# Optimization experiments

Measured on AMD Instinct MI355X. Metric: run time of the kernel, lower is better.

The kernel has to match this reference:

```python
import jax, jax.numpy as jnp
import numpy as np

EPS = 1e-06

def _feature_map(x):
    # elu(x) + 1
    return jax.nn.elu(x) + 1.0

def setup_inputs() -> dict:
    key = jax.random.key(0)
    k1, k2, k3 = jax.random.split(key, 3)
    N, L, H, D = 4, 8192, 8, 128
    queries = jax.random.normal(k1, (N, L, H, D), dtype=jnp.float32)
    keys = jax.random.normal(k2, (N, L, H, D), dtype=jnp.float32)
    values = jax.random.normal(k3, (N, L, H, D), dtype=jnp.float32)
    threshold = jnp.array([0.1], dtype=jnp.float32)
    return {"queries": queries, "keys": keys, "values": values, "threshold": threshold}

def reference(queries, keys, values, threshold):
    Q = _feature_map(queries)            # [N,L,H,D]
    K = _feature_map(keys)               # [N,L,H,D]
    v_length = values.shape[1]
    v = values / v_length                # [N,L,H,V]
    KV = jnp.einsum('nshd,nshv->nhdv', K, v)            # [N,H,D,V]
    scores = jnp.einsum('nlhd,nhd->nlh', Q, K.sum(axis=1))  # [N,L,H]
    sparse = jnp.where(scores > threshold[0], scores, jnp.zeros_like(scores))
    Z = 1.0 / (sparse + EPS)             # [N,L,H]
    out = jnp.einsum('nlhd,nhdv,nlh->nlhv', Q, KV, Z) * v_length
    return out
```

## Files before the change

kernel.cpp:

```cpp
#include <hip/hip_runtime.h>
#include <stdint.h>


#define LSEQ 8192
#define NHD  1024

typedef __attribute__((ext_vector_type(4))) float f32x4;
typedef __attribute__((ext_vector_type(8))) short bf16x8;
typedef unsigned short ushort_t;

static __device__ __forceinline__ unsigned short f2bf(float x) {
  union { float f; uint32_t u; } v; v.f = x;
  uint32_t r = v.u + 0x7FFFu + ((v.u >> 16) & 1u);
  return (unsigned short)(r >> 16);
}
static __device__ __forceinline__ uint32_t pack_bf(float a, float b) {
  return (uint32_t)f2bf(a) | ((uint32_t)f2bf(b) << 16);
}
static __device__ __forceinline__ float featmap(float x) {
  return x > 0.f ? x + 1.f : __expf(x);
}

#define LPAD 136

__global__ __launch_bounds__(512) void kv_direct(const float* __restrict__ keys,
                                                 const float* __restrict__ values,
                                                 float* __restrict__ kvp,
                                                 float* __restrict__ kspart) {
  __shared__ float kls[32 * LPAD];
  __shared__ float vls[32 * LPAD];
  const int tid = threadIdx.x;
  const int chunk = blockIdx.x, CH = gridDim.x;
  const int h = blockIdx.y, n = blockIdx.z, nh = n * 8 + h;
  const int lane = tid & 63, w = tid >> 6;
  const int wr = w >> 2, wc = w & 3;
  const int lr = lane & 15, lg = lane >> 4;
  const int sPer = LSEQ / CH;
  const int steps = sPer / 32;

  const size_t gb = ((size_t)n * LSEQ + (size_t)chunk * sPer) * NHD + h * 128;
  const float* gk = keys + gb;
  const float* gv = values + gb;

  const int srow = tid >> 5;
  const int c4 = tid & 31;

  f32x4 acc[4][2] = {};
  f32x4 ak[4] = {};
  bf16x8 ones;
  { uint32_t* u = (uint32_t*)&ones; u[0] = u[1] = u[2] = u[3] = 0x3F803F80u; }

  float4 kr[2], vr[2];
#pragma unroll
  for (int it = 0; it < 2; ++it) {
    size_t off = (size_t)(it * 16 + srow) * NHD + c4 * 4;
    kr[it] = *(const float4*)(gk + off);
    vr[it] = *(const float4*)(gv + off);
  }

  for (int t = 0; t < steps; ++t) {
#pragma unroll
    for (int it = 0; it < 2; ++it) {
      int s = it * 16 + srow;
      float4 kf = kr[it];
      kf.x = featmap(kf.x); kf.y = featmap(kf.y);
      kf.z = featmap(kf.z); kf.w = featmap(kf.w);
      *(float4*)&kls[s * LPAD + c4 * 4] = kf;
      *(float4*)&vls[s * LPAD + c4 * 4] = vr[it];
    }
    __syncthreads();
    if (t + 1 < steps) {
#pragma unroll
      for (int it = 0; it < 2; ++it) {
        size_t off = (size_t)((t + 1) * 32 + it * 16 + srow) * NHD + c4 * 4;
        kr[it] = *(const float4*)(gk + off);
        vr[it] = *(const float4*)(gv + off);
      }
    }
    bf16x8 af[4], bfr[2];
#pragma unroll
    for (int fr = 0; fr < 4; ++fr) {
      int d = wr * 64 + fr * 16 + lr;
      float f[8];
#pragma unroll
      for (int j = 0; j < 8; ++j) f[j] = kls[(lg * 8 + j) * LPAD + d];
      uint32_t* u = (uint32_t*)&af[fr];
      u[0] = pack_bf(f[0], f[1]); u[1] = pack_bf(f[2], f[3]);
      u[2] = pack_bf(f[4], f[5]); u[3] = pack_bf(f[6], f[7]);
    }
#pragma unroll
    for (int fc = 0; fc < 2; ++fc) {
      int v = wc * 32 + fc * 16 + lr;
      float f[8];
#pragma unroll
      for (int j = 0; j < 8; ++j) f[j] = vls[(lg * 8 + j) * LPAD + v];
      uint32_t* u = (uint32_t*)&bfr[fc];
      u[0] = pack_bf(f[0], f[1]); u[1] = pack_bf(f[2], f[3]);
      u[2] = pack_bf(f[4], f[5]); u[3] = pack_bf(f[6], f[7]);
    }
#pragma unroll
    for (int fr = 0; fr < 4; ++fr)
#pragma unroll
      for (int fc = 0; fc < 2; ++fc)
        acc[fr][fc] = __builtin_amdgcn_mfma_f32_16x16x32_bf16(af[fr], bfr[fc], acc[fr][fc], 0, 0, 0);
    if (wc == 0) {
#pragma unroll
      for (int fr = 0; fr < 4; ++fr)
        ak[fr] = __builtin_amdgcn_mfma_f32_16x16x32_bf16(af[fr], ones, ak[fr], 0, 0, 0);
    }
    __syncthreads();
  }

  float* dst = kvp + ((size_t)chunk * 32 + nh) * 16384;
#pragma unroll
  for (int fr = 0; fr < 4; ++fr)
#pragma unroll
    for (int fc = 0; fc < 2; ++fc) {
      int d0 = wr * 64 + fr * 16 + lg * 4;
      int v  = wc * 32 + fc * 16 + lr;
      *(float4*)(dst + (size_t)v * 128 + d0) =
          make_float4(acc[fr][fc][0], acc[fr][fc][1], acc[fr][fc][2], acc[fr][fc][3]);
    }
  if (wc == 0 && lr == 0) {
    float* ks = kspart + ((size_t)chunk * 32 + nh) * 128;
#pragma unroll
    for (int fr = 0; fr < 4; ++fr)
      *(float4*)(ks + wr * 64 + fr * 16 + lg * 4) =
          make_float4(ak[fr][0], ak[fr][1], ak[fr][2], ak[fr][3]);
  }
}

__global__ __launch_bounds__(256) void kv_merge(const float* __restrict__ kvp,
                                                const float* __restrict__ kspart,
                                                ushort_t* __restrict__ kvb,
                                                float* __restrict__ ksumg,
                                                int CH) {
  const int nh = blockIdx.x, q = blockIdx.y, tid = threadIdx.x;
  const size_t off = (size_t)nh * 16384 + q * 4096;
#pragma unroll
  for (int i = 0; i < 4; ++i) {
    size_t idx = off + (size_t)(i * 256 + tid) * 4;
    f32x4 s = {};
    for (int c = 0; c < CH; ++c)
      s += *(const f32x4*)(kvp + (size_t)c * 524288 + idx);
    *(uint2*)(kvb + idx) = make_uint2(pack_bf(s[0], s[1]), pack_bf(s[2], s[3]));
  }
  if (q == 0 && tid < 128) {
    float s = 0.f;
    for (int c = 0; c < CH; ++c) s += kspart[((size_t)c * 32 + nh) * 128 + tid];
    ksumg[nh * 128 + tid] = s;
  }
}

__global__ __launch_bounds__(256, 4) void attn_out(const float* __restrict__ q,
                                                   const ushort_t* __restrict__ kvb,
                                                   const float* __restrict__ ksumg,
                                                   const float* __restrict__ thrp,
                                                   float* __restrict__ out) {
  __shared__ __align__(16) uint32_t As[128 * 17 * 4];
  __shared__ float zrow[128];

  const int tid = threadIdx.x;
  const int mc = blockIdx.x, nh = blockIdx.y;
  const int n = nh >> 3, h = nh & 7;
  const size_t qoff = ((size_t)(n * LSEQ + mc * 128)) * NHD + h * 128;
  const float thr = thrp[0];

  const int c4 = tid & 31;
  const float4 kk = *(const float4*)(ksumg + nh * 128 + c4 * 4);

#pragma unroll
  for (int it = 0; it < 16; ++it) {
    int rr = it * 8 + (tid >> 5);
    float4 qv = *(const float4*)(q + qoff + (size_t)rr * NHD + c4 * 4);
    float f0 = featmap(qv.x), f1 = featmap(qv.y), f2 = featmap(qv.z), f3 = featmap(qv.w);
    uint32_t* dst = &As[(rr * 17 + (c4 >> 1)) * 4 + (c4 & 1) * 2];
    dst[0] = pack_bf(f0, f1);
    dst[1] = pack_bf(f2, f3);
    float p = f0 * kk.x + f1 * kk.y + f2 * kk.z + f3 * kk.w;
    p += __shfl_xor(p, 1);  p += __shfl_xor(p, 2);  p += __shfl_xor(p, 4);
    p += __shfl_xor(p, 8);  p += __shfl_xor(p, 16);
    if (c4 == 0) {
      float sp = p > thr ? p : 0.f;
      zrow[rr] = 1.f / (sp + 1e-6f);
    }
  }
  __syncthreads();

  const int lane = tid & 63;
  const int w = tid >> 6;
  const int lr = lane & 15, lg = lane >> 4;
  const ushort_t* kvp = kvb + (size_t)nh * 16384;

  f32x4 acc0[8] = {};
  f32x4 acc1[8] = {};
#pragma unroll
  for (int ks = 0; ks < 4; ++ks) {
    const int c8 = ks * 4 + lg;
    const int dof = ks * 32 + lg * 8;
    const int r0 = w * 32 + lr;
    bf16x8 a0 = *(const bf16x8*)&As[(r0 * 17 + c8) * 4];
    bf16x8 a1 = *(const bf16x8*)&As[((r0 + 16) * 17 + c8) * 4];
#pragma unroll
    for (int ct = 0; ct < 8; ++ct) {
      bf16x8 bb = *(const bf16x8*)(kvp + (size_t)((ct * 16 + lr) * 128) + dof);
      acc0[ct] = __builtin_amdgcn_mfma_f32_16x16x32_bf16(a0, bb, acc0[ct], 0, 0, 0);
      acc1[ct] = __builtin_amdgcn_mfma_f32_16x16x32_bf16(a1, bb, acc1[ct], 0, 0, 0);
    }
  }

  float z0[4], z1[4];
#pragma unroll
  for (int j = 0; j < 4; ++j) {
    z0[j] = zrow[w * 32 + lg * 4 + j];
    z1[j] = zrow[w * 32 + 16 + lg * 4 + j];
  }
  float* op = out + qoff;
#pragma unroll
  for (int ct = 0; ct < 8; ++ct)
#pragma unroll
    for (int jj = 0; jj < 4; ++jj) {
      int row = w * 32 + lg * 4 + jj;
      op[(size_t)row * NHD + ct * 16 + lr]        = acc0[ct][jj] * z0[jj];
      op[(size_t)(row + 16) * NHD + ct * 16 + lr] = acc1[ct][jj] * z1[jj];
    }
}

extern "C" void kernel_launch(void* const* d_in, const int* in_sizes, int n_in,
                              void* d_out, int out_size, void* d_ws, size_t ws_size,
                              hipStream_t stream) {
  const float* queries   = (const float*)d_in[0];
  const float* keys      = (const float*)d_in[1];
  const float* values    = (const float*)d_in[2];
  const float* threshold = (const float*)d_in[3];
  float* out = (float*)d_out;

  int CH = 16;
  while (CH > 1 &&
         (size_t)CH * (524288 + 32 * 128) * 4 + (size_t)32 * 16384 * 2 + 32 * 128 * 4 > ws_size)
    CH >>= 1;
  float* kvp     = (float*)d_ws;
  float* kspart  = kvp + (size_t)CH * 524288;
  ushort_t* kvb  = (ushort_t*)(kspart + (size_t)CH * 32 * 128);
  float* ksumg   = (float*)(kvb + (size_t)32 * 16384);

  kv_direct<<<dim3(CH, 8, 4), 512, 0, stream>>>(keys, values, kvp, kspart);
  kv_merge<<<dim3(32, 4), 256, 0, stream>>>(kvp, kspart, kvb, ksumg, CH);
  attn_out<<<dim3(64, 32), 256, 0, stream>>>(queries, kvb, ksumg, threshold, out);
}
```

Baseline: 193.9 us.

## Store K/V tiles in LDS as pre-packed transposed bf16 with XOR swizzle

The K/V tiles are now converted to bf16 and transposed (feature-major) before being written to shared memory. An XOR swizzle and padded stride are meant to avoid bank conflicts. Each MFMA operand then comes from a single 16-byte LDS read instead of eight scalar float reads plus per-lane packing, which halves LDS footprint and cuts LDS instructions and redundant conversions. Global loads change from float4 to float2 per thread, which may slightly reduce load efficiency.

```diff
diff --git a/kernel.cpp b/kernel.cpp
--- a/kernel.cpp
+++ b/kernel.cpp
@@ -4,6 +4,7 @@
 
 #define LSEQ 8192
 #define NHD  1024
+#define SP   20
 
 typedef __attribute__((ext_vector_type(4))) float f32x4;
 typedef __attribute__((ext_vector_type(8))) short bf16x8;
@@ -21,14 +22,12 @@
   return x > 0.f ? x + 1.f : __expf(x);
 }
 
-#define LPAD 136
-
 __global__ __launch_bounds__(512) void kv_direct(const float* __restrict__ keys,
                                                  const float* __restrict__ values,
                                                  float* __restrict__ kvp,
                                                  float* __restrict__ kspart) {
-  __shared__ float kls[32 * LPAD];
-  __shared__ float vls[32 * LPAD];
+  __shared__ uint32_t kls[128 * SP];
+  __shared__ uint32_t vls[128 * SP];
   const int tid = threadIdx.x;
   const int chunk = blockIdx.x, CH = gridDim.x;
   const int h = blockIdx.y, n = blockIdx.z, nh = n * 8 + h;
@@ -42,61 +41,59 @@
   const float* gk = keys + gb;
   const float* gv = values + gb;
 
-  const int srow = tid >> 5;
-  const int c4 = tid & 31;
+  const int a = lane;
+  const int wslot = (2 * w) ^ (((a >> 1) & 3) << 2);
+  const int wbase0 = (2 * a) * SP + wslot;
+  const int wbase1 = (2 * a + 1) * SP + wslot;
+
+  float2 kr[4], vr[4];
+#pragma unroll
+  for (int j = 0; j < 4; ++j) {
+    size_t off = (size_t)(4 * w + j) * NHD + 2 * a;
+    kr[j] = *(const float2*)(gk + off);
+    vr[j] = *(const float2*)(gv + off);
+  }
 
   f32x4 acc[4][2] = {};
   f32x4 ak[4] = {};
   bf16x8 ones;
   { uint32_t* u = (uint32_t*)&ones; u[0] = u[1] = u[2] = u[3] = 0x3F803F80u; }
 
-  float4 kr[2], vr[2];
-#pragma unroll
-  for (int it = 0; it < 2; ++it) {
-    size_t off = (size_t)(it * 16 + srow) * NHD + c4 * 4;
-    kr[it] = *(const float4*)(gk + off);
-    vr[it] = *(const float4*)(gv + off);
-  }
-
   for (int t = 0; t < steps; ++t) {
-#pragma unroll
-    for (int it = 0; it < 2; ++it) {
-      int s = it * 16 + srow;
-      float4 kf = kr[it];
-      kf.x = featmap(kf.x); kf.y = featmap(kf.y);
-      kf.z = featmap(kf.z); kf.w = featmap(kf.w);
-      *(float4*)&kls[s * LPAD + c4 * 4] = kf;
-      *(float4*)&vls[s * LPAD + c4 * 4] = vr[it];
+    {
+      uint2 kd0, kd1, vd0, vd1;
+      kd0.x = pack_bf(featmap(kr[0].x), featmap(kr[1].x));
+      kd0.y = pack_bf(featmap(kr[2].x), featmap(kr[3].x));
+      kd1.x = pack_bf(featmap(kr[0].y), featmap(kr[1].y));
+      kd1.y = pack_bf(featmap(kr[2].y), featmap(kr[3].y));
+      vd0.x = pack_bf(vr[0].x, vr[1].x);
+      vd0.y = pack_bf(vr[2].x, vr[3].x);
+      vd1.x = pack_bf(vr[0].y, vr[1].y);
+      vd1.y = pack_bf(vr[2].y, vr[3].y);
+      *(uint2*)&kls[wbase0] = kd0;
+      *(uint2*)&kls[wbase1] = kd1;
+      *(uint2*)&vls[wbase0] = vd0;
+      *(uint2*)&vls[wbase1] = vd1;
     }
     __syncthreads();
     if (t + 1 < steps) {
 #pragma unroll
-      for (int it = 0; it < 2; ++it) {
-        size_t off = (size_t)((t + 1) * 32 + it * 16 + srow) * NHD + c4 * 4;
-        kr[it] = *(const float4*)(gk + off);
-        vr[it] = *(const float4*)(gv + off);
+      for (int j = 0; j < 4; ++j) {
+        size_t off = (size_t)((t + 1) * 32 + 4 * w + j) * NHD + 2 * a;
+        kr[j] = *(const float2*)(gk + off);
+        vr[j] = *(const float2*)(gv + off);
       }
     }
     bf16x8 af[4], bfr[2];
 #pragma unroll
     for (int fr = 0; fr < 4; ++fr) {
       int d = wr * 64 + fr * 16 + lr;
-      float f[8];
-#pragma unroll
-      for (int j = 0; j < 8; ++j) f[j] = kls[(lg * 8 + j) * LPAD + d];
-      uint32_t* u = (uint32_t*)&af[fr];
-      u[0] = pack_bf(f[0], f[1]); u[1] = pack_bf(f[2], f[3]);
-      u[2] = pack_bf(f[4], f[5]); u[3] = pack_bf(f[6], f[7]);
+      af[fr] = *(const bf16x8*)&kls[d * SP + ((4 * lg) ^ ((((d >> 2)) & 3) << 2))];
     }
 #pragma unroll
     for (int fc = 0; fc < 2; ++fc) {
       int v = wc * 32 + fc * 16 + lr;
-      float f[8];
-#pragma unroll
-      for (int j = 0; j < 8; ++j) f[j] = vls[(lg * 8 + j) * LPAD + v];
-      uint32_t* u = (uint32_t*)&bfr[fc];
-      u[0] = pack_bf(f[0], f[1]); u[1] = pack_bf(f[2], f[3]);
-      u[2] = pack_bf(f[4], f[5]); u[3] = pack_bf(f[6], f[7]);
+      bfr[fc] = *(const bf16x8*)&vls[v * SP + ((4 * lg) ^ ((((v >> 2)) & 3) << 2))];
     }
 #pragma unroll
     for (int fr = 0; fr < 4; ++fr)
```

After: 176.0 us. -9.2%, faster.
